# Performance work log

Measured on AMD Instinct MI355X. Metric: run time of the kernel, lower is better.

Reference implementation:

```python
import jax, jax.numpy as jnp
import numpy as np

B, S, D = 4, 4096, 512

def setup_inputs() -> dict:
    key = jax.random.key(0)
    k1, k2, k3, k4 = jax.random.split(key, 4)
    return {
        "query": jax.random.normal(k1, (B, S, D), dtype=jnp.float32),
        "key": jax.random.normal(k2, (B, S, D), dtype=jnp.float32),
        "value": jax.random.normal(k3, (B, S, D), dtype=jnp.float32),
        "mask": jax.random.normal(k4, (1, S, S), dtype=jnp.float32),
    }

def reference(query, key, value, mask):
    dim = query.shape[-1]
    # scores: [B, S, S]
    scores = jnp.einsum("bqd,bkd->bqk", query, key) / jnp.sqrt(jnp.asarray(dim, query.dtype))
    scores = scores + mask  # additive mask, broadcast over batch
    attn = jax.nn.softmax(scores, axis=-1)
    return jnp.einsum("bqk,bkd->bqd", attn, value)
```

## Files before the change

### kernel.cpp

```cpp
#include <hip/hip_runtime.h>

#define S_LEN 4096
#define DHEAD 512
#define NBATCH 4
#define SCALE 0.044194173824159216f
#define PROW_PAD 76

typedef float f32x4 __attribute__((ext_vector_type(4)));
typedef short short8 __attribute__((ext_vector_type(8)));
typedef unsigned int uint2v __attribute__((ext_vector_type(2)));

static __device__ __forceinline__ unsigned int pk2(float a, float b) {
  union { __bf16 h[2]; unsigned int u; } t;
  t.h[0] = (__bf16)a; t.h[1] = (__bf16)b;
  return t.u;
}

static __device__ __forceinline__ void gload16(const void* g, void* l) {
  __builtin_amdgcn_global_load_lds((const __attribute__((address_space(1))) void*)g,
                                   (__attribute__((address_space(3))) void*)l, 16, 0, 0);
}

__global__ void cvt_k_kernel(const float* __restrict__ K, unsigned short* __restrict__ KB) {
  const size_t i = ((size_t)blockIdx.x * 256 + threadIdx.x) * 8;
  f32x4 a = *(const f32x4*)(K + i);
  f32x4 b = *(const f32x4*)(K + i + 4);
  union { unsigned int u[4]; f32x4 q; } o;
  o.u[0] = pk2(a[0], a[1]); o.u[1] = pk2(a[2], a[3]);
  o.u[2] = pk2(b[0], b[1]); o.u[3] = pk2(b[2], b[3]);
  *(f32x4*)(KB + i) = o.q;
}

#define TP_PAD 76
__global__ void transpose_v_kernel(const float* __restrict__ V, unsigned short* __restrict__ VT) {
  __shared__ unsigned short t[64 * TP_PAD];
  const int tid = (int)threadIdx.x;
  const int bx = (int)blockIdx.x;
  const int b = bx >> 9, rem = bx & 511, st = rem >> 3, dt = rem & 7;
  const int s0 = st << 6, d0 = dt << 6;
  const float* Vb = V + (size_t)b * S_LEN * DHEAD;
  unsigned short* Tb = VT + (size_t)b * DHEAD * S_LEN;
  {
    const int sp = (tid >> 3) << 1;
    const int d8 = (tid & 7) << 3;
    const float* p0 = Vb + (size_t)(s0 + sp) * DHEAD + d0 + d8;
    f32x4 a0 = *(const f32x4*)(p0);
    f32x4 a1 = *(const f32x4*)(p0 + 4);
    f32x4 b0 = *(const f32x4*)(p0 + DHEAD);
    f32x4 b1 = *(const f32x4*)(p0 + DHEAD + 4);
    #pragma unroll
    for (int j = 0; j < 4; ++j) {
      *(unsigned int*)&t[(d8 + j) * TP_PAD + sp]     = pk2(a0[j], b0[j]);
      *(unsigned int*)&t[(d8 + 4 + j) * TP_PAD + sp] = pk2(a1[j], b1[j]);
    }
  }
  __syncthreads();
  {
    const int d = tid >> 2, sq = (tid & 3) << 4;
    union { uint2v h[2]; f32x4 q; } u0, u1;
    u0.h[0] = *(const uint2v*)&t[d * TP_PAD + sq];
    u0.h[1] = *(const uint2v*)&t[d * TP_PAD + sq + 4];
    u1.h[0] = *(const uint2v*)&t[d * TP_PAD + sq + 8];
    u1.h[1] = *(const uint2v*)&t[d * TP_PAD + sq + 12];
    f32x4* out = (f32x4*)(Tb + (size_t)(d0 + d) * S_LEN + s0 + sq);
    out[0] = u0.q; out[1] = u1.q;
  }
}

struct __align__(16) SmemV3 {
  unsigned short kt[64 * 512];
  unsigned short vt[512 * 64];
  unsigned short pt[64 * PROW_PAD];
  float halfmax[2][64];
  float halfsum[2][64];
  float fct[64];
  float lsum[64];
};

__global__ __launch_bounds__(512, 2)
void lightning_attn_v3(const float* __restrict__ Q, const unsigned short* __restrict__ KB,
                       const unsigned short* __restrict__ VT, const float* __restrict__ M,
                       float* __restrict__ O)
{
  __shared__ SmemV3 sm;
  const int tid = (int)threadIdx.x;
  const int l = tid & 63;
  const int w = tid >> 6;
  const int g = l >> 4;
  const int c = l & 15;
  const int qgrp = w & 3;
  const int khalf = w >> 2;

  const int bid = (int)blockIdx.x;
  const int b = bid >> 6;
  const int q0 = (bid & 63) * 64;

  const float* Qb = Q + (size_t)b * S_LEN * DHEAD;
  const unsigned short* Kb = KB + (size_t)b * S_LEN * DHEAD;
  const unsigned short* Vb = VT + (size_t)b * DHEAD * S_LEN;

  short8 qf[16];
  {
    const float* qp = Qb + (size_t)(q0 + qgrp*16 + c) * DHEAD;
    #pragma unroll
    for (int ds = 0; ds < 16; ++ds) {
      const int d0 = ds*32 + g*8;
      f32x4 f0 = *(const f32x4*)(qp + d0);
      f32x4 f1 = *(const f32x4*)(qp + d0 + 4);
      union { unsigned int u[4]; short8 s; } pk;
      pk.u[0] = pk2(f0[0]*SCALE, f0[1]*SCALE);
      pk.u[1] = pk2(f0[2]*SCALE, f0[3]*SCALE);
      pk.u[2] = pk2(f1[0]*SCALE, f1[1]*SCALE);
      pk.u[3] = pk2(f1[2]*SCALE, f1[3]*SCALE);
      qf[ds] = pk.s;
    }
  }

  float m_run = -1e30f, l_run = 0.f;
  f32x4 oacc[4][4];
  #pragma unroll
  for (int qt = 0; qt < 4; ++qt)
    #pragma unroll
    for (int dt = 0; dt < 4; ++dt)
      oacc[qt][dt] = (f32x4){0.f, 0.f, 0.f, 0.f};

  for (int it = 0; it < S_LEN / 64; ++it) {
    const int k0 = it * 64;

    __syncthreads();

    const float* mrow = M + (size_t)(q0 + qgrp*16 + c) * S_LEN + (k0 + khalf*32 + g*4);
    f32x4 mk0 = *(const f32x4*)(mrow);
    f32x4 mk1 = *(const f32x4*)(mrow + 16);

    {
      const char* kg = (const char*)(Kb + (size_t)k0 * DHEAD);
      #pragma unroll
      for (int i = 0; i < 8; ++i) {
        const int p = tid + 512*i, r = p >> 6, ch = p & 63;
        gload16(kg + r*1024 + ((ch ^ (r & 7)) * 16), (char*)sm.kt + p*16);
      }
      #pragma unroll
      for (int i = 0; i < 8; ++i) {
        const int p = tid + 512*i, r = p >> 3, ch = p & 7;
        gload16((const char*)Vb + ((size_t)r * S_LEN + k0)*2 + ((ch ^ (r & 7)) * 16),
                (char*)sm.vt + p*16);
      }
    }
    __syncthreads();

    f32x4 acc0 = (f32x4){0,0,0,0}, acc1 = (f32x4){0,0,0,0};
    {
      const int rr = khalf*32 + c;
      const int x7 = rr & 7;
      const char* ka = (const char*)sm.kt + rr*1024;
      #pragma unroll
      for (int ds = 0; ds < 16; ++ds) {
        const int off = ((ds*4 + g) ^ x7) * 16;
        short8 a0 = *(const short8*)(ka + off);
        short8 a1 = *(const short8*)(ka + 16*1024 + off);
        acc0 = __builtin_amdgcn_mfma_f32_16x16x32_bf16(a0, qf[ds], acc0, 0, 0, 0);
        acc1 = __builtin_amdgcn_mfma_f32_16x16x32_bf16(a1, qf[ds], acc1, 0, 0, 0);
      }
    }

    float s0[4], s1[4];
    #pragma unroll
    for (int r = 0; r < 4; ++r) { s0[r] = acc0[r] + mk0[r]; s1[r] = acc1[r] + mk1[r]; }

    float pm = fmaxf(fmaxf(fmaxf(s0[0], s0[1]), fmaxf(s0[2], s0[3])),
                     fmaxf(fmaxf(s1[0], s1[1]), fmaxf(s1[2], s1[3])));
    pm = fmaxf(pm, __shfl_xor(pm, 16));
    pm = fmaxf(pm, __shfl_xor(pm, 32));
    if (l < 16) sm.halfmax[khalf][qgrp*16 + l] = pm;
    __syncthreads();

    const float mt = fmaxf(sm.halfmax[0][qgrp*16 + c], sm.halfmax[1][qgrp*16 + c]);
    const float m_new = fmaxf(m_run, mt);
    const float fac = __expf(m_run - m_new);
    m_run = m_new;

    float p0[4], p1[4]; float psum = 0.f;
    #pragma unroll
    for (int r = 0; r < 4; ++r) { p0[r] = __expf(s0[r] - m_new); psum += p0[r]; }
    #pragma unroll
    for (int r = 0; r < 4; ++r) { p1[r] = __expf(s1[r] - m_new); psum += p1[r]; }
    psum += __shfl_xor(psum, 16);
    psum += __shfl_xor(psum, 32);

    {
      unsigned short* pr = &sm.pt[(qgrp*16 + c) * PROW_PAD + khalf*32 + 4*g];
      uint2v pw0; pw0[0] = pk2(p0[0], p0[1]); pw0[1] = pk2(p0[2], p0[3]);
      uint2v pw1; pw1[0] = pk2(p1[0], p1[1]); pw1[1] = pk2(p1[2], p1[3]);
      *(uint2v*)(pr) = pw0;
      *(uint2v*)(pr + 16) = pw1;
    }
    if (l < 16) {
      sm.halfsum[khalf][qgrp*16 + l] = psum;
      if (khalf == 0) sm.fct[qgrp*16 + l] = fac;
    }
    __syncthreads();

    if (khalf == 0)
      l_run = l_run * fac + (psum + sm.halfsum[1][qgrp*16 + c]);

    #pragma unroll
    for (int qt = 0; qt < 4; ++qt) {
      f32x4 fv = *(const f32x4*)&sm.fct[qt*16 + 4*g];
      #pragma unroll
      for (int dt = 0; dt < 4; ++dt)
        #pragma unroll
        for (int r = 0; r < 4; ++r)
          oacc[qt][dt][r] *= fv[r];
    }

    #pragma unroll
    for (int kw = 0; kw < 2; ++kw) {
      short8 bfr[4];
      #pragma unroll
      for (int dt = 0; dt < 4; ++dt) {
        const int rv = w*64 + dt*16 + c;
        bfr[dt] = *(const short8*)((const char*)sm.vt + rv*128 + (((kw*4 + g) ^ (rv & 7)) * 16));
      }
      #pragma unroll
      for (int qt = 0; qt < 4; ++qt) {
        short8 af = *(const short8*)&sm.pt[(qt*16 + c) * PROW_PAD + kw*32 + 8*g];
        #pragma unroll
        for (int dt = 0; dt < 4; ++dt)
          oacc[qt][dt] = __builtin_amdgcn_mfma_f32_16x16x32_bf16(af, bfr[dt], oacc[qt][dt], 0, 0, 0);
      }
    }
  }

  if (khalf == 0 && l < 16) sm.lsum[qgrp*16 + l] = l_run;
  __syncthreads();
  {
    float* ob = O + ((size_t)b * S_LEN + q0) * DHEAD + w*64 + c;
    #pragma unroll
    for (int qt = 0; qt < 4; ++qt) {
      f32x4 lv = *(const f32x4*)&sm.lsum[qt*16 + 4*g];
      #pragma unroll
      for (int r = 0; r < 4; ++r) {
        const float inv = 1.0f / lv[r];
        float* orow = ob + (size_t)(qt*16 + 4*g + r) * DHEAD;
        #pragma unroll
        for (int dt = 0; dt < 4; ++dt)
          orow[dt*16] = oacc[qt][dt][r] * inv;
      }
    }
  }
}

#define KROW_PAD2 524
#define VROW_PAD2 76
struct __align__(16) SmemV2 {
  unsigned short kt[64 * KROW_PAD2];
  unsigned short vtT[512 * VROW_PAD2];
  unsigned short pt[64 * PROW_PAD];
  float halfmax[2][64];
  float halfsum[2][64];
  float fct[64];
  float lsum[64];
};

__global__ __launch_bounds__(512, 2)
void lightning_attn_v2(const float* __restrict__ Q, const float* __restrict__ K,
                       const float* __restrict__ V, const float* __restrict__ M,
                       float* __restrict__ O)
{
  __shared__ SmemV2 sm;
  const int tid = (int)threadIdx.x;
  const int l = tid & 63;
  const int w = tid >> 6;
  const int g = l >> 4;
  const int c = l & 15;
  const int qgrp = w & 3;
  const int khalf = w >> 2;
  const int bid = (int)blockIdx.x;
  const int b = bid >> 6;
  const int q0 = (bid & 63) * 64;
  const float* Qb = Q + (size_t)b * S_LEN * DHEAD;
  const float* Kb = K + (size_t)b * S_LEN * DHEAD;
  const float* Vb = V + (size_t)b * S_LEN * DHEAD;
  short8 qf[16];
  {
    const float* qp = Qb + (size_t)(q0 + qgrp*16 + c) * DHEAD;
    #pragma unroll
    for (int ds = 0; ds < 16; ++ds) {
      const int d0 = ds*32 + g*8;
      f32x4 f0 = *(const f32x4*)(qp + d0);
      f32x4 f1 = *(const f32x4*)(qp + d0 + 4);
      union { unsigned int u[4]; short8 s; } pk;
      pk.u[0] = pk2(f0[0]*SCALE, f0[1]*SCALE);
      pk.u[1] = pk2(f0[2]*SCALE, f0[3]*SCALE);
      pk.u[2] = pk2(f1[0]*SCALE, f1[1]*SCALE);
      pk.u[3] = pk2(f1[2]*SCALE, f1[3]*SCALE);
      qf[ds] = pk.s;
    }
  }
  float m_run = -1e30f, l_run = 0.f;
  f32x4 oacc[4][4];
  #pragma unroll
  for (int qt = 0; qt < 4; ++qt)
    #pragma unroll
    for (int dt = 0; dt < 4; ++dt)
      oacc[qt][dt] = (f32x4){0.f, 0.f, 0.f, 0.f};
  const int ks_row = tid >> 3, ks_cg = tid & 7;
  for (int it = 0; it < S_LEN / 64; ++it) {
    const int k0 = it * 64;
    const float* mrow = M + (size_t)(q0 + qgrp*16 + c) * S_LEN + (k0 + khalf*32 + g*4);
    f32x4 mk0 = *(const f32x4*)(mrow);
    f32x4 mk1 = *(const f32x4*)(mrow + 16);
    __syncthreads();
    {
      const float* kp = Kb + (size_t)(k0 + ks_row) * DHEAD;
      #pragma unroll 8
      for (int u = 0; u < 16; ++u) {
        const int d0 = (ks_cg + u*8) * 4;
        f32x4 f = *(const f32x4*)(kp + d0);
        uint2v pk; pk[0] = pk2(f[0], f[1]); pk[1] = pk2(f[2], f[3]);
        *(uint2v*)&sm.kt[ks_row * KROW_PAD2 + d0] = pk;
      }
    }
    {
      #pragma unroll
      for (int u = 0; u < 4; ++u) {
        const int blk = tid + 512*u;
        const int kblk = blk >> 7;
        const int dblk = blk & 127;
        const float* vp = Vb + (size_t)(k0 + kblk*4) * DHEAD + dblk*4;
        f32x4 f0 = *(const f32x4*)(vp);
        f32x4 f1 = *(const f32x4*)(vp + DHEAD);
        f32x4 f2 = *(const f32x4*)(vp + 2*DHEAD);
        f32x4 f3 = *(const f32x4*)(vp + 3*DHEAD);
        #pragma unroll
        for (int i = 0; i < 4; ++i) {
          uint2v o; o[0] = pk2(f0[i], f1[i]); o[1] = pk2(f2[i], f3[i]);
          *(uint2v*)&sm.vtT[(dblk*4 + i) * VROW_PAD2 + kblk*4] = o;
        }
      }
    }
    __syncthreads();
    f32x4 acc0 = (f32x4){0,0,0,0}, acc1 = (f32x4){0,0,0,0};
    {
      const unsigned short* ka = &sm.kt[(khalf*32 + c) * KROW_PAD2];
      #pragma unroll
      for (int ds = 0; ds < 16; ++ds) {
        const int dd = ds*32 + g*8;
        short8 a0 = *(const short8*)(ka + dd);
        short8 a1 = *(const short8*)(ka + 16*KROW_PAD2 + dd);
        acc0 = __builtin_amdgcn_mfma_f32_16x16x32_bf16(a0, qf[ds], acc0, 0, 0, 0);
        acc1 = __builtin_amdgcn_mfma_f32_16x16x32_bf16(a1, qf[ds], acc1, 0, 0, 0);
      }
    }
    float s0[4], s1[4];
    #pragma unroll
    for (int r = 0; r < 4; ++r) { s0[r] = acc0[r] + mk0[r]; s1[r] = acc1[r] + mk1[r]; }
    float pm = fmaxf(fmaxf(fmaxf(s0[0], s0[1]), fmaxf(s0[2], s0[3])),
                     fmaxf(fmaxf(s1[0], s1[1]), fmaxf(s1[2], s1[3])));
    pm = fmaxf(pm, __shfl_xor(pm, 16));
    pm = fmaxf(pm, __shfl_xor(pm, 32));
    if (l < 16) sm.halfmax[khalf][qgrp*16 + l] = pm;
    __syncthreads();
    const float mt = fmaxf(sm.halfmax[0][qgrp*16 + c], sm.halfmax[1][qgrp*16 + c]);
    const float m_new = fmaxf(m_run, mt);
    const float fac = __expf(m_run - m_new);
    m_run = m_new;
    float p0[4], p1[4]; float psum = 0.f;
    #pragma unroll
    for (int r = 0; r < 4; ++r) { p0[r] = __expf(s0[r] - m_new); psum += p0[r]; }
    #pragma unroll
    for (int r = 0; r < 4; ++r) { p1[r] = __expf(s1[r] - m_new); psum += p1[r]; }
    psum += __shfl_xor(psum, 16);
    psum += __shfl_xor(psum, 32);
    {
      unsigned short* pr = &sm.pt[(qgrp*16 + c) * PROW_PAD + khalf*32 + 4*g];
      uint2v pw0; pw0[0] = pk2(p0[0], p0[1]); pw0[1] = pk2(p0[2], p0[3]);
      uint2v pw1; pw1[0] = pk2(p1[0], p1[1]); pw1[1] = pk2(p1[2], p1[3]);
      *(uint2v*)(pr) = pw0;
      *(uint2v*)(pr + 16) = pw1;
    }
    if (l < 16) {
      sm.halfsum[khalf][qgrp*16 + l] = psum;
      if (khalf == 0) sm.fct[qgrp*16 + l] = fac;
    }
    __syncthreads();
    if (khalf == 0)
      l_run = l_run * fac + (psum + sm.halfsum[1][qgrp*16 + c]);
    #pragma unroll
    for (int qt = 0; qt < 4; ++qt) {
      f32x4 fv = *(const f32x4*)&sm.fct[qt*16 + 4*g];
      #pragma unroll
      for (int dt = 0; dt < 4; ++dt)
        #pragma unroll
        for (int r = 0; r < 4; ++r)
          oacc[qt][dt][r] *= fv[r];
    }
    #pragma unroll
    for (int kw = 0; kw < 2; ++kw) {
      short8 bfr[4];
      #pragma unroll
      for (int dt = 0; dt < 4; ++dt)
        bfr[dt] = *(const short8*)&sm.vtT[(w*64 + dt*16 + c) * VROW_PAD2 + kw*32 + 8*g];
      #pragma unroll
      for (int qt = 0; qt < 4; ++qt) {
        short8 af = *(const short8*)&sm.pt[(qt*16 + c) * PROW_PAD + kw*32 + 8*g];
        #pragma unroll
        for (int dt = 0; dt < 4; ++dt)
          oacc[qt][dt] = __builtin_amdgcn_mfma_f32_16x16x32_bf16(af, bfr[dt], oacc[qt][dt], 0, 0, 0);
      }
    }
  }
  if (khalf == 0 && l < 16) sm.lsum[qgrp*16 + l] = l_run;
  __syncthreads();
  {
    float* ob = O + ((size_t)b * S_LEN + q0) * DHEAD + w*64 + c;
    #pragma unroll
    for (int qt = 0; qt < 4; ++qt) {
      f32x4 lv = *(const f32x4*)&sm.lsum[qt*16 + 4*g];
      #pragma unroll
      for (int r = 0; r < 4; ++r) {
        const float inv = 1.0f / lv[r];
        float* orow = ob + (size_t)(qt*16 + 4*g + r) * DHEAD;
        #pragma unroll
        for (int dt = 0; dt < 4; ++dt)
          orow[dt*16] = oacc[qt][dt][r] * inv;
      }
    }
  }
}

extern "C" void kernel_launch(void* const* d_in, const int* in_sizes, int n_in,
                              void* d_out, int out_size, void* d_ws, size_t ws_size,
                              hipStream_t stream) {
  (void)in_sizes; (void)n_in; (void)out_size;
  const float* Q = (const float*)d_in[0];
  const float* K = (const float*)d_in[1];
  const float* V = (const float*)d_in[2];
  const float* M = (const float*)d_in[3];
  float* O = (float*)d_out;

  const size_t need = (size_t)2 * NBATCH * S_LEN * DHEAD * sizeof(unsigned short);
  if (ws_size >= need) {
    unsigned short* KB  = (unsigned short*)d_ws;
    unsigned short* VTg = KB + (size_t)NBATCH * S_LEN * DHEAD;
    cvt_k_kernel<<<4096, 256, 0, stream>>>(K, KB);
    transpose_v_kernel<<<NBATCH * 64 * 8, 256, 0, stream>>>(V, VTg);
    lightning_attn_v3<<<NBATCH * 64, 512, 0, stream>>>(Q, KB, VTg, M, O);
  } else {
    lightning_attn_v2<<<NBATCH * 64, 512, 0, stream>>>(Q, K, V, M, O);
  }
}
```

Before: 308.0 us.

## Restructure attention kernel: 4-way key split, K prefetch overlap, lazy rescale

Each wave now covers 32 queries and 16 keys instead of 16 queries and 32 keys, so every K fragment read from LDS feeds two MFMAs. The next K tile is loaded asynchronously after the softmax barrier so it overlaps the PV matmul, and V loads are issued before the QK compute. Each wave keeps its own partial row sum, so one shared-memory sum exchange per iteration goes away. The P buffer uses an XOR swizzle instead of padding, and the output rescale is skipped when every factor is 1. The costs are extra registers for the doubled Q fragments, a 4-way max reduction through LDS, and tighter ordering of the asynchronous loads.

```diff
diff --git a/kernel.cpp b/kernel.cpp
--- a/kernel.cpp
+++ b/kernel.cpp
@@ -4,7 +4,6 @@
 #define DHEAD 512
 #define NBATCH 4
 #define SCALE 0.044194173824159216f
-#define PROW_PAD 76
 
 typedef float f32x4 __attribute__((ext_vector_type(4)));
 typedef short short8 __attribute__((ext_vector_type(8)));
@@ -67,29 +66,30 @@
   }
 }
 
-struct __align__(16) SmemV3 {
+struct __align__(16) SmemV4 {
   unsigned short kt[64 * 512];
   unsigned short vt[512 * 64];
-  unsigned short pt[64 * PROW_PAD];
-  float halfmax[2][64];
-  float halfsum[2][64];
+  unsigned short pt[64 * 64];
+  float qmax[4][64];
   float fct[64];
+  float lpart[4][64];
   float lsum[64];
 };
 
 __global__ __launch_bounds__(512, 2)
-void lightning_attn_v3(const float* __restrict__ Q, const unsigned short* __restrict__ KB,
+void lightning_attn_v4(const float* __restrict__ Q, const unsigned short* __restrict__ KB,
                        const unsigned short* __restrict__ VT, const float* __restrict__ M,
                        float* __restrict__ O)
 {
-  __shared__ SmemV3 sm;
+  __shared__ SmemV4 sm;
   const int tid = (int)threadIdx.x;
   const int l = tid & 63;
   const int w = tid >> 6;
   const int g = l >> 4;
   const int c = l & 15;
-  const int qgrp = w & 3;
-  const int khalf = w >> 2;
+  const int qh = w & 1;
+  const int kq = w >> 1;
+  const int x7 = c & 7;
 
   const int bid = (int)blockIdx.x;
   const int b = bid >> 6;
@@ -99,24 +99,32 @@
   const unsigned short* Kb = KB + (size_t)b * S_LEN * DHEAD;
   const unsigned short* Vb = VT + (size_t)b * DHEAD * S_LEN;
 
-  short8 qf[16];
-  {
-    const float* qp = Qb + (size_t)(q0 + qgrp*16 + c) * DHEAD;
+  short8 qf0[16], qf1[16];
+  {
+    const float* qp0 = Qb + (size_t)(q0 + qh*32 + c) * DHEAD;
+    const float* qp1 = qp0 + 16 * DHEAD;
     #pragma unroll
     for (int ds = 0; ds < 16; ++ds) {
       const int d0 = ds*32 + g*8;
-      f32x4 f0 = *(const f32x4*)(qp + d0);
-      f32x4 f1 = *(const f32x4*)(qp + d0 + 4);
+      f32x4 f0 = *(const f32x4*)(qp0 + d0);
+      f32x4 f1 = *(const f32x4*)(qp0 + d0 + 4);
       union { unsigned int u[4]; short8 s; } pk;
       pk.u[0] = pk2(f0[0]*SCALE, f0[1]*SCALE);
       pk.u[1] = pk2(f0[2]*SCALE, f0[3]*SCALE);
       pk.u[2] = pk2(f1[0]*SCALE, f1[1]*SCALE);
       pk.u[3] = pk2(f1[2]*SCALE, f1[3]*SCALE);
-      qf[ds] = pk.s;
-    }
-  }
-
-  float m_run = -1e30f, l_run = 0.f;
+      qf0[ds] = pk.s;
+      f0 = *(const f32x4*)(qp1 + d0);
+      f1 = *(const f32x4*)(qp1 + d0 + 4);
+      pk.u[0] = pk2(f0[0]*SCALE, f0[1]*SCALE);
+      pk.u[1] = pk2(f0[2]*SCALE, f0[3]*SCALE);
+      pk.u[2] = pk2(f1[0]*SCALE, f1[1]*SCALE);
+      pk.u[3] = pk2(f1[2]*SCALE, f1[3]*SCALE);
+      qf1[ds] = pk.s;
+    }
+  }
+
+  float m0 = -1e30f, m1 = -1e30f, lr0 = 0.f, lr1 = 0.f;
   f32x4 oacc[4][4];
   #pragma unroll
   for (int qt = 0; qt < 4; ++qt)
@@ -124,115 +132,149 @@
     for (int dt = 0; dt < 4; ++dt)
       oacc[qt][dt] = (f32x4){0.f, 0.f, 0.f, 0.f};
 
+  {
+    const char* kg = (const char*)Kb;
+    #pragma unroll
+    for (int i = 0; i < 8; ++i) {
+      const int p = tid + 512*i, r = p >> 6, ch = p & 63;
+      gload16(kg + r*1024 + ((ch ^ (r & 7)) * 16), (char*)sm.kt + p*16);
+    }
+  }
+  __syncthreads();
+
   for (int it = 0; it < S_LEN / 64; ++it) {
     const int k0 = it * 64;
 
-    __syncthreads();
-
-    const float* mrow = M + (size_t)(q0 + qgrp*16 + c) * S_LEN + (k0 + khalf*32 + g*4);
+    const float* mrow = M + (size_t)(q0 + qh*32 + c) * S_LEN + (k0 + kq*16 + g*4);
     f32x4 mk0 = *(const f32x4*)(mrow);
-    f32x4 mk1 = *(const f32x4*)(mrow + 16);
-
-    {
-      const char* kg = (const char*)(Kb + (size_t)k0 * DHEAD);
+    f32x4 mk1 = *(const f32x4*)(mrow + 16 * S_LEN);
+
+    #pragma unroll
+    for (int i = 0; i < 8; ++i) {
+      const int p = tid + 512*i, r = p >> 3, ch = p & 7;
+      gload16((const char*)Vb + ((size_t)r * S_LEN + k0)*2 + ((ch ^ (r & 7)) * 16),
+              (char*)sm.vt + p*16);
+    }
+
+    f32x4 acc0 = (f32x4){0,0,0,0}, acc1 = (f32x4){0,0,0,0};
+    {
+      const char* ka = (const char*)sm.kt + (kq*16 + c)*1024;
+      #pragma unroll
+      for (int ds = 0; ds < 16; ++ds) {
+        short8 a = *(const short8*)(ka + (((ds*4 + g) ^ x7) * 16));
+        acc0 = __builtin_amdgcn_mfma_f32_16x16x32_bf16(a, qf0[ds], acc0, 0, 0, 0);
+        acc1 = __builtin_amdgcn_mfma_f32_16x16x32_bf16(a, qf1[ds], acc1, 0, 0, 0);
+      }
+    }
+
+    float s0[4], s1[4];
+    #pragma unroll
+    for (int r = 0; r < 4; ++r) { s0[r] = acc0[r] + mk0[r]; s1[r] = acc1[r] + mk1[r]; }
+
+    float pm0 = fmaxf(fmaxf(s0[0], s0[1]), fmaxf(s0[2], s0[3]));
+    float pm1 = fmaxf(fmaxf(s1[0], s1[1]), fmaxf(s1[2], s1[3]));
+    pm0 = fmaxf(pm0, __shfl_xor(pm0, 16)); pm0 = fmaxf(pm0, __shfl_xor(pm0, 32));
+    pm1 = fmaxf(pm1, __shfl_xor(pm1, 16)); pm1 = fmaxf(pm1, __shfl_xor(pm1, 32));
+    if (l < 16) {
+      sm.qmax[kq][qh*32 + l]      = pm0;
+      sm.qmax[kq][qh*32 + 16 + l] = pm1;
+    }
+    asm volatile("s_waitcnt lgkmcnt(0)" ::: "memory");
+    __builtin_amdgcn_s_barrier();
+    asm volatile("" ::: "memory");
+
+    float mx0 = sm.qmax[g][qh*32 + c];
+    float mx1 = sm.qmax[g][qh*32 + 16 + c];
+    mx0 = fmaxf(mx0, __shfl_xor(mx0, 16)); mx0 = fmaxf(mx0, __shfl_xor(mx0, 32));
+    mx1 = fmaxf(mx1, __shfl_xor(mx1, 16)); mx1 = fmaxf(mx1, __shfl_xor(mx1, 32));
+
+    const float mn0 = fmaxf(m0, mx0), mn1 = fmaxf(m1, mx1);
+    const float fac0 = __expf(m0 - mn0), fac1 = __expf(m1 - mn1);
+    m0 = mn0; m1 = mn1;
+
+    float p0[4], p1[4]; float ps0 = 0.f, ps1 = 0.f;
+    #pragma unroll
+    for (int r = 0; r < 4; ++r) { p0[r] = __expf(s0[r] - mn0); ps0 += p0[r]; }
+    #pragma unroll
+    for (int r = 0; r < 4; ++r) { p1[r] = __expf(s1[r] - mn1); ps1 += p1[r]; }
+    ps0 += __shfl_xor(ps0, 16); ps0 += __shfl_xor(ps0, 32);
+    ps1 += __shfl_xor(ps1, 16); ps1 += __shfl_xor(ps1, 32);
+    lr0 = lr0 * fac0 + ps0;
+    lr1 = lr1 * fac1 + ps1;
+
+    {
+      const int chB = (2*kq + (g>>1)) * 16;
+      const int sub = 8*(g&1);
+      uint2v pw;
+      pw[0] = pk2(p0[0], p0[1]); pw[1] = pk2(p0[2], p0[3]);
+      *(uint2v*)((char*)sm.pt + (qh*32 + c)*128 + ((chB ^ (x7*16))) + sub) = pw;
+      pw[0] = pk2(p1[0], p1[1]); pw[1] = pk2(p1[2], p1[3]);
+      *(uint2v*)((char*)sm.pt + (qh*32 + 16 + c)*128 + ((chB ^ (x7*16))) + sub) = pw;
+    }
+    if (kq == 0 && l < 16) {
+      sm.fct[qh*32 + l]      = fac0;
+      sm.fct[qh*32 + 16 + l] = fac1;
+    }
+    __syncthreads();
+
+    if (it < S_LEN/64 - 1) {
+      const char* kg = (const char*)Kb + (size_t)(k0 + 64) * 1024;
       #pragma unroll
       for (int i = 0; i < 8; ++i) {
         const int p = tid + 512*i, r = p >> 6, ch = p & 63;
         gload16(kg + r*1024 + ((ch ^ (r & 7)) * 16), (char*)sm.kt + p*16);
       }
-      #pragma unroll
-      for (int i = 0; i < 8; ++i) {
-        const int p = tid + 512*i, r = p >> 3, ch = p & 7;
-        gload16((const char*)Vb + ((size_t)r * S_LEN + k0)*2 + ((ch ^ (r & 7)) * 16),
-                (char*)sm.vt + p*16);
-      }
-    }
-    __syncthreads();
-
-    f32x4 acc0 = (f32x4){0,0,0,0}, acc1 = (f32x4){0,0,0,0};
-    {
-      const int rr = khalf*32 + c;
-      const int x7 = rr & 7;
-      const char* ka = (const char*)sm.kt + rr*1024;
-      #pragma unroll
-      for (int ds = 0; ds < 16; ++ds) {
-        const int off = ((ds*4 + g) ^ x7) * 16;
-        short8 a0 = *(const short8*)(ka + off);
-        short8 a1 = *(const short8*)(ka + 16*1024 + off);
-        acc0 = __builtin_amdgcn_mfma_f32_16x16x32_bf16(a0, qf[ds], acc0, 0, 0, 0);
-        acc1 = __builtin_amdgcn_mfma_f32_16x16x32_bf16(a1, qf[ds], acc1, 0, 0, 0);
-      }
-    }
-
-    float s0[4], s1[4];
-    #pragma unroll
-    for (int r = 0; r < 4; ++r) { s0[r] = acc0[r] + mk0[r]; s1[r] = acc1[r] + mk1[r]; }
-
-    float pm = fmaxf(fmaxf(fmaxf(s0[0], s0[1]), fmaxf(s0[2], s0[3])),
-                     fmaxf(fmaxf(s1[0], s1[1]), fmaxf(s1[2], s1[3])));
-    pm = fmaxf(pm, __shfl_xor(pm, 16));
-    pm = fmaxf(pm, __shfl_xor(pm, 32));
-    if (l < 16) sm.halfmax[khalf][qgrp*16 + l] = pm;
-    __syncthreads();
-
-    const float mt = fmaxf(sm.halfmax[0][qgrp*16 + c], sm.halfmax[1][qgrp*16 + c]);
-    const float m_new = fmaxf(m_run, mt);
-    const float fac = __expf(m_run - m_new);
-    m_run = m_new;
-
-    float p0[4], p1[4]; float psum = 0.f;
-    #pragma unroll
-    for (int r = 0; r < 4; ++r) { p0[r] = __expf(s0[r] - m_new); psum += p0[r]; }
-    #pragma unroll
-    for (int r = 0; r < 4; ++r) { p1[r] = __expf(s1[r] - m_new); psum += p1[r]; }
-    psum += __shfl_xor(psum, 16);
-    psum += __shfl_xor(psum, 32);
-
-    {
-      unsigned short* pr = &sm.pt[(qgrp*16 + c) * PROW_PAD + khalf*32 + 4*g];
-      uint2v pw0; pw0[0] = pk2(p0[0], p0[1]); pw0[1] = pk2(p0[2], p0[3]);
-      uint2v pw1; pw1[0] = pk2(p1[0], p1[1]); pw1[1] = pk2(p1[2], p1[3]);
-      *(uint2v*)(pr) = pw0;
-      *(uint2v*)(pr + 16) = pw1;
-    }
-    if (l < 16) {
-      sm.halfsum[khalf][qgrp*16 + l] = psum;
-      if (khalf == 0) sm.fct[qgrp*16 + l] = fac;
-    }
-    __syncthreads();
-
-    if (khalf == 0)
-      l_run = l_run * fac + (psum + sm.halfsum[1][qgrp*16 + c]);
-
-    #pragma unroll
-    for (int qt = 0; qt < 4; ++qt) {
-      f32x4 fv = *(const f32x4*)&sm.fct[qt*16 + 4*g];
+    }
+
+    {
+      f32x4 fv0 = *(const f32x4*)&sm.fct[0*16 + 4*g];
+      f32x4 fv1 = *(const f32x4*)&sm.fct[1*16 + 4*g];
+      f32x4 fv2 = *(const f32x4*)&sm.fct[2*16 + 4*g];
+      f32x4 fv3 = *(const f32x4*)&sm.fct[3*16 + 4*g];
+      int one = (fv0[0]==1.f)&(fv0[1]==1.f)&(fv0[2]==1.f)&(fv0[3]==1.f)
+              & (fv1[0]==1.f)&(fv1[1]==1.f)&(fv1[2]==1.f)&(fv1[3]==1.f)
+              & (fv2[0]==1.f)&(fv2[1]==1.f)&(fv2[2]==1.f)&(fv2[3]==1.f)
+              & (fv3[0]==1.f)&(fv3[1]==1.f)&(fv3[2]==1.f)&(fv3[3]==1.f);
+      if (!__all(one)) {
+        #pragma unroll
+        for (int dt = 0; dt < 4; ++dt) {
+          #pragma unroll
+          for (int r = 0; r < 4; ++r) {
+            oacc[0][dt][r] *= fv0[r];
+            oacc[1][dt][r] *= fv1[r];
+            oacc[2][dt][r] *= fv2[r];
+            oacc[3][dt][r] *= fv3[r];
+          }
+        }
+      }
+    }
+
+    #pragma unroll
+    for (int ks = 0; ks < 2; ++ks) {
+      const int chk = ((ks*4 + g) ^ x7) * 16;
+      short8 bv[4], pf[4];
       #pragma unroll
       for (int dt = 0; dt < 4; ++dt)
-        #pragma unroll
-        for (int r = 0; r < 4; ++r)
-          oacc[qt][dt][r] *= fv[r];
-    }
-
-    #pragma unroll
-    for (int kw = 0; kw < 2; ++kw) {
-      short8 bfr[4];
-      #pragma unroll
-      for (int dt = 0; dt < 4; ++dt) {
-        const int rv = w*64 + dt*16 + c;
-        bfr[dt] = *(const short8*)((const char*)sm.vt + rv*128 + (((kw*4 + g) ^ (rv & 7)) * 16));
-      }
-      #pragma unroll
-      for (int qt = 0; qt < 4; ++qt) {
-        short8 af = *(const short8*)&sm.pt[(qt*16 + c) * PROW_PAD + kw*32 + 8*g];
+        bv[dt] = *(const short8*)((const char*)sm.vt + (w*64 + dt*16 + c)*128 + chk);
+      #pragma unroll
+      for (int qt = 0; qt < 4; ++qt)
+        pf[qt] = *(const short8*)((const char*)sm.pt + (qt*16 + c)*128 + chk);
+      #pragma unroll
+      for (int qt = 0; qt < 4; ++qt)
         #pragma unroll
         for (int dt = 0; dt < 4; ++dt)
-          oacc[qt][dt] = __builtin_amdgcn_mfma_f32_16x16x32_bf16(af, bfr[dt], oacc[qt][dt], 0, 0, 0);
-      }
-    }
-  }
-
-  if (khalf == 0 && l < 16) sm.lsum[qgrp*16 + l] = l_run;
+          oacc[qt][dt] = __builtin_amdgcn_mfma_f32_16x16x32_bf16(pf[qt], bv[dt], oacc[qt][dt], 0, 0, 0);
+    }
+    __syncthreads();
+  }
+
+  if (l < 16) {
+    sm.lpart[kq][qh*32 + l]      = lr0;
+    sm.lpart[kq][qh*32 + 16 + l] = lr1;
+  }
+  __syncthreads();
+  if (tid < 64)
+    sm.lsum[tid] = sm.lpart[0][tid] + sm.lpart[1][tid] + sm.lpart[2][tid] + sm.lpart[3][tid];
   __syncthreads();
   {
     float* ob = O + ((size_t)b * S_LEN + q0) * DHEAD + w*64 + c;
@@ -253,6 +295,7 @@
 
 #define KROW_PAD2 524
 #define VROW_PAD2 76
+#define PROW_PAD 76
 struct __align__(16) SmemV2 {
   unsigned short kt[64 * KROW_PAD2];
   unsigned short vtT[512 * VROW_PAD2];
@@ -442,11 +485,11 @@
 
   const size_t need = (size_t)2 * NBATCH * S_LEN * DHEAD * sizeof(unsigned short);
   if (ws_size >= need) {
-    unsigned short* KB  = (unsigned short*)d_ws;
-    unsigned short* VTg = KB + (size_t)NBATCH * S_LEN * DHEAD;
-    cvt_k_kernel<<<4096, 256, 0, stream>>>(K, KB);
-    transpose_v_kernel<<<NBATCH * 64 * 8, 256, 0, stream>>>(V, VTg);
-    lightning_attn_v3<<<NBATCH * 64, 512, 0, stream>>>(Q, KB, VTg, M, O);
+    unsigned short* KBp = (unsigned short*)d_ws;
+    unsigned short* VTp = KBp + (size_t)NBATCH * S_LEN * DHEAD;
+    cvt_k_kernel<<<4096, 256, 0, stream>>>(K, KBp);
+    transpose_v_kernel<<<NBATCH * 64 * 8, 256, 0, stream>>>(V, VTp);
+    lightning_attn_v4<<<NBATCH * 64, 512, 0, stream>>>(Q, KBp, VTp, M, O);
   } else {
     lightning_attn_v2<<<NBATCH * 64, 512, 0, stream>>>(Q, K, V, M, O);
   }
```

New measurement: 529.2 us. 1.72x slower.

## Double-buffer K tiles, read V from global into registers, convert mask to bf16

Applied to the files above, without the earlier changes.

Splits the shared K tile into two buffers and prefetches the next K tile during the softmax/PV phase, which removes one barrier per iteration. V^T fragments now load straight from global into registers instead of being staged in LDS. The additive mask is first converted to bf16 in a separate kernel, halving its per-iteration read traffic, at the cost of an extra conversion pass over the 4096x4096 mask and reduced mask precision. Register pressure rises from the bvr fragments, and the direct global V reads rely on cache hits.

```diff
diff --git a/kernel.cpp b/kernel.cpp
--- a/kernel.cpp
+++ b/kernel.cpp
@@ -15,20 +15,25 @@
   t.h[0] = (__bf16)a; t.h[1] = (__bf16)b;
   return t.u;
 }
-
+static __device__ __forceinline__ float blo(unsigned int u) {
+  union { unsigned int x; float f; } t; t.x = u << 16; return t.f;
+}
+static __device__ __forceinline__ float bhi(unsigned int u) {
+  union { unsigned int x; float f; } t; t.x = u & 0xffff0000u; return t.f;
+}
 static __device__ __forceinline__ void gload16(const void* g, void* l) {
   __builtin_amdgcn_global_load_lds((const __attribute__((address_space(1))) void*)g,
                                    (__attribute__((address_space(3))) void*)l, 16, 0, 0);
 }
 
-__global__ void cvt_k_kernel(const float* __restrict__ K, unsigned short* __restrict__ KB) {
+__global__ void cvt_bf16_kernel(const float* __restrict__ X, unsigned short* __restrict__ XB) {
   const size_t i = ((size_t)blockIdx.x * 256 + threadIdx.x) * 8;
-  f32x4 a = *(const f32x4*)(K + i);
-  f32x4 b = *(const f32x4*)(K + i + 4);
+  f32x4 a = *(const f32x4*)(X + i);
+  f32x4 b = *(const f32x4*)(X + i + 4);
   union { unsigned int u[4]; f32x4 q; } o;
   o.u[0] = pk2(a[0], a[1]); o.u[1] = pk2(a[2], a[3]);
   o.u[2] = pk2(b[0], b[1]); o.u[3] = pk2(b[2], b[3]);
-  *(f32x4*)(KB + i) = o.q;
+  *(f32x4*)(XB + i) = o.q;
 }
 
 #define TP_PAD 76
@@ -67,9 +72,8 @@
   }
 }
 
-struct __align__(16) SmemV3 {
-  unsigned short kt[64 * 512];
-  unsigned short vt[512 * 64];
+struct __align__(16) SmemV7 {
+  unsigned short kt[2][64 * 512];
   unsigned short pt[64 * PROW_PAD];
   float halfmax[2][64];
   float halfsum[2][64];
@@ -78,11 +82,11 @@
 };
 
 __global__ __launch_bounds__(512, 2)
-void lightning_attn_v3(const float* __restrict__ Q, const unsigned short* __restrict__ KB,
-                       const unsigned short* __restrict__ VT, const float* __restrict__ M,
+void lightning_attn_v7(const float* __restrict__ Q, const unsigned short* __restrict__ KB,
+                       const unsigned short* __restrict__ VT, const unsigned short* __restrict__ MB,
                        float* __restrict__ O)
 {
-  __shared__ SmemV3 sm;
+  __shared__ SmemV7 sm;
   const int tid = (int)threadIdx.x;
   const int l = tid & 63;
   const int w = tid >> 6;
@@ -124,36 +128,39 @@
     for (int dt = 0; dt < 4; ++dt)
       oacc[qt][dt] = (f32x4){0.f, 0.f, 0.f, 0.f};
 
+  const unsigned short* vb0 = Vb + (size_t)(w*64 + c) * S_LEN + 8*g;
+
+  {
+    const char* kg = (const char*)Kb;
+    #pragma unroll
+    for (int i = 0; i < 8; ++i) {
+      const int p = tid + 512*i, r = p >> 6, ch = p & 63;
+      gload16(kg + r*1024 + ((ch ^ (r & 7)) * 16), (char*)sm.kt[0] + p*16);
+    }
+  }
+
   for (int it = 0; it < S_LEN / 64; ++it) {
     const int k0 = it * 64;
-
-    __syncthreads();
-
-    const float* mrow = M + (size_t)(q0 + qgrp*16 + c) * S_LEN + (k0 + khalf*32 + g*4);
-    f32x4 mk0 = *(const f32x4*)(mrow);
-    f32x4 mk1 = *(const f32x4*)(mrow + 16);
-
-    {
-      const char* kg = (const char*)(Kb + (size_t)k0 * DHEAD);
-      #pragma unroll
-      for (int i = 0; i < 8; ++i) {
-        const int p = tid + 512*i, r = p >> 6, ch = p & 63;
-        gload16(kg + r*1024 + ((ch ^ (r & 7)) * 16), (char*)sm.kt + p*16);
-      }
-      #pragma unroll
-      for (int i = 0; i < 8; ++i) {
-        const int p = tid + 512*i, r = p >> 3, ch = p & 7;
-        gload16((const char*)Vb + ((size_t)r * S_LEN + k0)*2 + ((ch ^ (r & 7)) * 16),
-                (char*)sm.vt + p*16);
-      }
-    }
+    const int cur = it & 1;
+
+    const unsigned short* mrow = MB + (size_t)(q0 + qgrp*16 + c) * S_LEN + (k0 + khalf*32 + g*4);
+    uint2v mu0 = *(const uint2v*)(mrow);
+    uint2v mu1 = *(const uint2v*)(mrow + 16);
+
+    short8 bvr[2][4];
+    #pragma unroll
+    for (int kw = 0; kw < 2; ++kw)
+      #pragma unroll
+      for (int dt = 0; dt < 4; ++dt)
+        bvr[kw][dt] = *(const short8*)(vb0 + (size_t)(dt*16) * S_LEN + k0 + kw*32);
+
     __syncthreads();
 
     f32x4 acc0 = (f32x4){0,0,0,0}, acc1 = (f32x4){0,0,0,0};
     {
       const int rr = khalf*32 + c;
       const int x7 = rr & 7;
-      const char* ka = (const char*)sm.kt + rr*1024;
+      const char* ka = (const char*)sm.kt[cur] + rr*1024;
       #pragma unroll
       for (int ds = 0; ds < 16; ++ds) {
         const int off = ((ds*4 + g) ^ x7) * 16;
@@ -165,8 +172,10 @@
     }
 
     float s0[4], s1[4];
-    #pragma unroll
-    for (int r = 0; r < 4; ++r) { s0[r] = acc0[r] + mk0[r]; s1[r] = acc1[r] + mk1[r]; }
+    s0[0] = acc0[0] + blo(mu0[0]); s0[1] = acc0[1] + bhi(mu0[0]);
+    s0[2] = acc0[2] + blo(mu0[1]); s0[3] = acc0[3] + bhi(mu0[1]);
+    s1[0] = acc1[0] + blo(mu1[0]); s1[1] = acc1[1] + bhi(mu1[0]);
+    s1[2] = acc1[2] + blo(mu1[1]); s1[3] = acc1[3] + bhi(mu1[1]);
 
     float pm = fmaxf(fmaxf(fmaxf(s0[0], s0[1]), fmaxf(s0[2], s0[3])),
                      fmaxf(fmaxf(s1[0], s1[1]), fmaxf(s1[2], s1[3])));
@@ -204,6 +213,15 @@
     if (khalf == 0)
       l_run = l_run * fac + (psum + sm.halfsum[1][qgrp*16 + c]);
 
+    if (it < S_LEN/64 - 1) {
+      const char* kg = (const char*)Kb + (size_t)(k0 + 64) * 1024;
+      #pragma unroll
+      for (int i = 0; i < 8; ++i) {
+        const int p = tid + 512*i, r = p >> 6, ch = p & 63;
+        gload16(kg + r*1024 + ((ch ^ (r & 7)) * 16), (char*)sm.kt[cur^1] + p*16);
+      }
+    }
+
     #pragma unroll
     for (int qt = 0; qt < 4; ++qt) {
       f32x4 fv = *(const f32x4*)&sm.fct[qt*16 + 4*g];
@@ -216,18 +234,12 @@
 
     #pragma unroll
     for (int kw = 0; kw < 2; ++kw) {
-      short8 bfr[4];
-      #pragma unroll
-      for (int dt = 0; dt < 4; ++dt) {
-        const int rv = w*64 + dt*16 + c;
-        bfr[dt] = *(const short8*)((const char*)sm.vt + rv*128 + (((kw*4 + g) ^ (rv & 7)) * 16));
-      }
       #pragma unroll
       for (int qt = 0; qt < 4; ++qt) {
         short8 af = *(const short8*)&sm.pt[(qt*16 + c) * PROW_PAD + kw*32 + 8*g];
         #pragma unroll
         for (int dt = 0; dt < 4; ++dt)
-          oacc[qt][dt] = __builtin_amdgcn_mfma_f32_16x16x32_bf16(af, bfr[dt], oacc[qt][dt], 0, 0, 0);
+          oacc[qt][dt] = __builtin_amdgcn_mfma_f32_16x16x32_bf16(af, bvr[kw][dt], oacc[qt][dt], 0, 0, 0);
       }
     }
   }
@@ -440,13 +452,17 @@
   const float* M = (const float*)d_in[3];
   float* O = (float*)d_out;
 
-  const size_t need = (size_t)2 * NBATCH * S_LEN * DHEAD * sizeof(unsigned short);
-  if (ws_size >= need) {
-    unsigned short* KB  = (unsigned short*)d_ws;
-    unsigned short* VTg = KB + (size_t)NBATCH * S_LEN * DHEAD;
-    cvt_k_kernel<<<4096, 256, 0, stream>>>(K, KB);
-    transpose_v_kernel<<<NBATCH * 64 * 8, 256, 0, stream>>>(V, VTg);
-    lightning_attn_v3<<<NBATCH * 64, 512, 0, stream>>>(Q, KB, VTg, M, O);
+  const size_t szKV = (size_t)NBATCH * S_LEN * DHEAD * sizeof(unsigned short);
+  const size_t szM  = (size_t)S_LEN * S_LEN * sizeof(unsigned short);
+
+  if (ws_size >= 2 * szKV + szM) {
+    unsigned short* KBp = (unsigned short*)d_ws;
+    unsigned short* VTp = KBp + (size_t)NBATCH * S_LEN * DHEAD;
+    unsigned short* MBp = VTp + (size_t)NBATCH * S_LEN * DHEAD;
+    cvt_bf16_kernel<<<4096, 256, 0, stream>>>(K, KBp);
+    transpose_v_kernel<<<NBATCH * 64 * 8, 256, 0, stream>>>(V, VTp);
+    cvt_bf16_kernel<<<8192, 256, 0, stream>>>(M, MBp);
+    lightning_attn_v7<<<NBATCH * 64, 512, 0, stream>>>(Q, KBp, VTp, MBp, O);
   } else {
     lightning_attn_v2<<<NBATCH * 64, 512, 0, stream>>>(Q, K, V, M, O);
   }
```

Result: slower. 346.2 us (+12.4%).
